# Kernel tuning notes

Hardware: AMD Instinct MI355X
Metric: run time of the kernel (lower is better)

## Reference

```python
import jax, jax.numpy as jnp
from jax import lax
import numpy as np

N_E = 1024
E_DIM = 512
BETA = 0.25


def setup_inputs() -> dict:
    key = jax.random.key(0)
    k1, k2 = jax.random.split(key)
    z = jax.random.normal(k1, (16, 4096, E_DIM), dtype=jnp.float32)
    # torch init: uniform(-1/n_e, 1/n_e)
    codebook = jax.random.uniform(k2, (N_E, E_DIM), dtype=jnp.float32,
                                  minval=-1.0 / N_E, maxval=1.0 / N_E)
    return {"z": z, "codebook": codebook}


def reference(z, codebook):
    zf = z.reshape(-1, z.shape[-1])                      # (N, e_dim)
    # squared-distance matrix: ||z||^2 + ||e||^2 - 2 z e^T  -> (N, n_e)
    d = (jnp.sum(zf * zf, axis=1, keepdims=True)
         + jnp.sum(codebook * codebook, axis=1)
         - 2.0 * (zf @ codebook.T))
    idx = jnp.argmin(d, axis=1)                          # (N,)
    z_q = codebook[idx].reshape(z.shape)                 # (B, S, e_dim)
    loss = (jnp.mean((z_q - lax.stop_gradient(z)) ** 2)
            + BETA * jnp.mean((lax.stop_gradient(z_q) - z) ** 2))
    # straight-through estimator
    z_q_st = z + lax.stop_gradient(z_q - z)
    # perplexity of code usage (mean of one-hot == normalized counts)
    counts = jnp.zeros((codebook.shape[0],), dtype=z.dtype).at[idx].add(1.0)
    e_mean = counts / idx.shape[0]
    perplexity = jnp.exp(-jnp.sum(e_mean * jnp.log(e_mean + 1e-10)))
    return (loss, z_q_st, idx, perplexity)
```

## Files before the change

### kernel.cpp

```cpp
#include <hip/hip_runtime.h>
#include <hip/hip_bf16.h>

#define N_ROWS 65536
#define EDIM   512
#define NCODES 1024

#define WS_LOSS   0
#define WS_COUNTS 1
#define WS_ENORM  1025
#define WS_ZNORM  2049
#define WS_AMBCNT (2049 + 65536)
#define WS_WINNER (WS_AMBCNT + 1)
#define WS_AMBLST (WS_WINNER + 65536)
#define AMB_CAP   32768
#define WS_E2_OFF (1u << 20)
#define WS_FAST_BYTES (3u * 1024u * 1024u + 4096u)

#define AMB_EPS 1.6e-4f

typedef short short8 __attribute__((ext_vector_type(8)));
typedef float f32x4  __attribute__((ext_vector_type(4)));

#define AS1C(p) ((const __attribute__((address_space(1))) void*)(p))
#define AS3(p)  ((__attribute__((address_space(3))) void*)(p))

static __device__ __forceinline__ unsigned short f2bf(float f) {
    unsigned u = __float_as_uint(f);
    u += 0x7FFFu + ((u >> 16) & 1u);
    return (unsigned short)(u >> 16);
}
static __device__ __forceinline__ float bf2f(unsigned short h) {
    return __uint_as_float(((unsigned)h) << 16);
}

__global__ __launch_bounds__(256) void vq_prep(const float* __restrict__ cb,
                                               float* __restrict__ ws) {
    int j = blockIdx.x;
    int tid = threadIdx.x;
    float2 v = *(const float2*)&cb[(size_t)j * EDIM + tid * 2];
    float s = v.x * v.x + v.y * v.y;
    #pragma unroll
    for (int off = 32; off > 0; off >>= 1) s += __shfl_down(s, off);
    __shared__ float ls[4];
    int wave = tid >> 6, lane = tid & 63;
    if (lane == 0) ls[wave] = s;
    __syncthreads();
    if (tid == 0) {
        ws[WS_ENORM + j] = ls[0] + ls[1] + ls[2] + ls[3];
        ws[WS_COUNTS + j] = 0.0f;
        if (j == 0) {
            ws[WS_LOSS] = 0.0f;
            ((int*)ws)[WS_AMBCNT] = 0;
        }
    }
}

__global__ __launch_bounds__(256) void vq_znorm(const float* __restrict__ z,
                                                float* __restrict__ ws) {
    int tid  = threadIdx.x;
    int lrow = tid >> 5;
    int c    = tid & 31;
    long row = (long)blockIdx.x * 8 + lrow;
    const float* p = z + row * EDIM + (c >> 3) * 128 + (c & 7);
    float r = p[0] * p[0];
    #pragma unroll
    for (int i = 1; i < 16; ++i) {
        float v = p[i * 8];
        r += v * v;
    }
    r += __shfl_xor(r, 1);
    r += __shfl_xor(r, 2);
    r += __shfl_xor(r, 4);
    r += __shfl_xor(r, 8);
    r += __shfl_xor(r, 16);
    if (c == 0) ws[WS_ZNORM + row] = r;
}

__global__ __launch_bounds__(256) void vq_convz(const float* __restrict__ z,
                                                unsigned short* __restrict__ z2) {
    const int tid = threadIdx.x;
    const int p = blockIdx.x;
    const long row0 = (long)p * 128;
    const int row = tid >> 1, half = tid & 1;
    for (int kc = 0; kc < 16; ++kc) {
        const float* src = z + (row0 + row) * EDIM + kc * 32 + half * 16;
        float f[16];
        #pragma unroll
        for (int q = 0; q < 4; ++q) {
            float4 v = ((const float4*)src)[q];
            f[q*4+0] = v.x; f[q*4+1] = v.y; f[q*4+2] = v.z; f[q*4+3] = v.w;
        }
        unsigned hi[8], lo[8];
        #pragma unroll
        for (int q = 0; q < 8; ++q) {
            unsigned short h0 = f2bf(f[2*q]);
            unsigned short h1 = f2bf(f[2*q+1]);
            unsigned short l0 = f2bf(f[2*q]   - bf2f(h0));
            unsigned short l1 = f2bf(f[2*q+1] - bf2f(h1));
            hi[q] = (unsigned)h0 | ((unsigned)h1 << 16);
            lo[q] = (unsigned)l0 | ((unsigned)l1 << 16);
        }
        size_t base = ((size_t)(p * 16 + kc) * 2) * 4096;
        unsigned* dhi = (unsigned*)(z2 + base        + row * 32 + half * 16);
        unsigned* dlo = (unsigned*)(z2 + base + 4096 + row * 32 + half * 16);
        ((uint4*)dhi)[0] = make_uint4(hi[0], hi[1], hi[2], hi[3]);
        ((uint4*)dhi)[1] = make_uint4(hi[4], hi[5], hi[6], hi[7]);
        ((uint4*)dlo)[0] = make_uint4(lo[0], lo[1], lo[2], lo[3]);
        ((uint4*)dlo)[1] = make_uint4(lo[4], lo[5], lo[6], lo[7]);
    }
}

__global__ __launch_bounds__(256) void vq_convcb(const float* __restrict__ cb,
                                                 unsigned short* __restrict__ e2) {
    const int tid = threadIdx.x;
    const int cc = blockIdx.x;
    const int row = tid >> 1, half = tid & 1;
    for (int kc = 0; kc < 16; ++kc) {
        const float* src = cb + (size_t)(cc * 128 + row) * EDIM + kc * 32 + half * 16;
        float f[16];
        #pragma unroll
        for (int q = 0; q < 4; ++q) {
            float4 v = ((const float4*)src)[q];
            f[q*4+0] = v.x; f[q*4+1] = v.y; f[q*4+2] = v.z; f[q*4+3] = v.w;
        }
        unsigned hi[8], lo[8];
        #pragma unroll
        for (int q = 0; q < 8; ++q) {
            unsigned short h0 = f2bf(f[2*q]);
            unsigned short h1 = f2bf(f[2*q+1]);
            unsigned short l0 = f2bf(f[2*q]   - bf2f(h0));
            unsigned short l1 = f2bf(f[2*q+1] - bf2f(h1));
            hi[q] = (unsigned)h0 | ((unsigned)h1 << 16);
            lo[q] = (unsigned)l0 | ((unsigned)l1 << 16);
        }
        size_t base = ((size_t)(cc * 16 + kc) * 2) * 4096;
        unsigned* dhi = (unsigned*)(e2 + base        + row * 32 + half * 16);
        unsigned* dlo = (unsigned*)(e2 + base + 4096 + row * 32 + half * 16);
        ((uint4*)dhi)[0] = make_uint4(hi[0], hi[1], hi[2], hi[3]);
        ((uint4*)dhi)[1] = make_uint4(hi[4], hi[5], hi[6], hi[7]);
        ((uint4*)dlo)[0] = make_uint4(lo[0], lo[1], lo[2], lo[3]);
        ((uint4*)dlo)[1] = make_uint4(lo[4], lo[5], lo[6], lo[7]);
    }
}

__device__ __forceinline__ void stage32(const char* zs, const char* es,
                                        char* db, int goff, int w) {
    const int wb = w << 10;
    #pragma unroll
    for (int i = 0; i < 4; ++i) {
        __builtin_amdgcn_global_load_lds(AS1C(zs + goff + i * 2048),
                                         AS3(db + i * 4096 + wb), 16, 0, 0);
        __builtin_amdgcn_global_load_lds(AS1C(es + goff + i * 2048),
                                         AS3(db + 16384 + i * 4096 + wb), 16, 0, 0);
    }
}

__global__ __launch_bounds__(256, 2) void vq_mfma(const unsigned short* __restrict__ z2,
                                                  const unsigned short* __restrict__ e2,
                                                  const float* __restrict__ ws,
                                                  int* __restrict__ winner,
                                                  int* __restrict__ amb_count,
                                                  int* __restrict__ amb_list) {
    __shared__ __attribute__((aligned(16))) char sb[2][32768];
    __shared__ float enorm_lds[NCODES];
    __shared__ float fv1[2][128];
    __shared__ float fv2[2][128];
    __shared__ int   fc1[2][128];

    const int tid  = threadIdx.x;
    const int lane = tid & 63, w = tid >> 6;
    const int rw   = (w & 1) * 64;
    const int wcol = w >> 1;
    const int cw   = wcol * 64;
    const int ml = lane & 15, kg = lane >> 4;
    const long row0 = (long)blockIdx.x * 128;

    const int t3 = tid >> 3;
    const int sl = (tid & 7) ^ (t3 & 7);
    const int goff = t3 * 64 + (sl & 3) * 16 + (sl >> 2) * 8192;

    const int xr = ml & 7;
    const int o0 = (kg ^ xr) * 16;
    const int o1 = ((4 + kg) ^ xr) * 16;
    const int za = (rw + ml) * 128;
    const int ea = 16384 + (cw + ml) * 128;

    #pragma unroll
    for (int i = 0; i < 4; ++i) enorm_lds[tid + i * 256] = ws[WS_ENORM + tid + i * 256];

    float v1[16], v2[16];
    int   c1[16];
    #pragma unroll
    for (int i = 0; i < 16; ++i) { v1[i] = INFINITY; v2[i] = INFINITY; c1[i] = 0; }

    const char* z2b = (const char*)z2 + (size_t)blockIdx.x * 16 * 16384;
    const char* e2b = (const char*)e2;

    f32x4 acc[4][4];
    #pragma unroll
    for (int rt = 0; rt < 4; ++rt)
        #pragma unroll
        for (int ct = 0; ct < 4; ++ct)
            acc[rt][ct] = (f32x4){0.f, 0.f, 0.f, 0.f};

    stage32(z2b, e2b, sb[0], goff, w);
    __syncthreads();

    int cur = 0;
    #pragma unroll 2
    for (int s = 0; s < 128; ++s) {
        if (s + 1 < 128) {
            const int s2 = s + 1;
            stage32(z2b + (size_t)(s2 & 15) * 16384,
                    e2b + (size_t)s2 * 16384,
                    sb[cur ^ 1], goff, w);
        }
        const char* bz = sb[cur];
        short8 a[4][2], b[4][2];
        #pragma unroll
        for (int rt = 0; rt < 4; ++rt) {
            a[rt][0] = *(const short8*)(bz + za + rt * 2048 + o0);
            a[rt][1] = *(const short8*)(bz + za + rt * 2048 + o1);
        }
        #pragma unroll
        for (int ct = 0; ct < 4; ++ct) {
            b[ct][0] = *(const short8*)(bz + ea + ct * 2048 + o0);
            b[ct][1] = *(const short8*)(bz + ea + ct * 2048 + o1);
        }
        #pragma unroll
        for (int rt = 0; rt < 4; ++rt)
            #pragma unroll
            for (int ct = 0; ct < 4; ++ct) {
                acc[rt][ct] = __builtin_amdgcn_mfma_f32_16x16x32_bf16(a[rt][0], b[ct][0], acc[rt][ct], 0, 0, 0);
                acc[rt][ct] = __builtin_amdgcn_mfma_f32_16x16x32_bf16(a[rt][0], b[ct][1], acc[rt][ct], 0, 0, 0);
                acc[rt][ct] = __builtin_amdgcn_mfma_f32_16x16x32_bf16(a[rt][1], b[ct][0], acc[rt][ct], 0, 0, 0);
            }
        asm volatile("s_waitcnt vmcnt(0)" ::: "memory");
        __builtin_amdgcn_s_barrier();
        asm volatile("" ::: "memory");
        cur ^= 1;

        if ((s & 15) == 15) {
            const int cc = s >> 4;
            #pragma unroll
            for (int ct = 0; ct < 4; ++ct) {
                const int code = cc * 128 + cw + ct * 16 + ml;
                const float en = enorm_lds[code];
                #pragma unroll
                for (int rt = 0; rt < 4; ++rt)
                    #pragma unroll
                    for (int reg = 0; reg < 4; ++reg) {
                        float d = fmaf(-2.0f, acc[rt][ct][reg], en);
                        int i = rt * 4 + reg;
                        bool lt1 = d < v1[i];
                        bool lt2 = d < v2[i];
                        v2[i] = lt1 ? v1[i] : (lt2 ? d : v2[i]);
                        v1[i] = lt1 ? d : v1[i];
                        c1[i] = lt1 ? code : c1[i];
                    }
            }
            #pragma unroll
            for (int rt = 0; rt < 4; ++rt)
                #pragma unroll
                for (int ct = 0; ct < 4; ++ct)
                    acc[rt][ct] = (f32x4){0.f, 0.f, 0.f, 0.f};
        }
    }

    #pragma unroll
    for (int i = 0; i < 16; ++i) {
        #pragma unroll
        for (int off = 1; off < 16; off <<= 1) {
            float ov1 = __shfl_xor(v1[i], off);
            int   oc1 = __shfl_xor(c1[i], off);
            float ov2 = __shfl_xor(v2[i], off);
            bool take = (ov1 < v1[i]) || (ov1 == v1[i] && oc1 < c1[i]);
            float nv2 = take ? fminf(v1[i], ov2) : fminf(v2[i], ov1);
            v1[i] = take ? ov1 : v1[i];
            c1[i] = take ? oc1 : c1[i];
            v2[i] = nv2;
        }
    }
    __syncthreads();
    if (ml == 0) {
        #pragma unroll
        for (int i = 0; i < 16; ++i) {
            int row = rw + (i >> 2) * 16 + kg * 4 + (i & 3);
            fv1[wcol][row] = v1[i];
            fv2[wcol][row] = v2[i];
            fc1[wcol][row] = c1[i];
        }
    }
    __syncthreads();
    if (tid < 128) {
        float a1 = fv1[0][tid], a2 = fv2[0][tid];
        int   ac = fc1[0][tid];
        float b1 = fv1[1][tid], b2 = fv2[1][tid];
        int   bc = fc1[1][tid];
        bool take = (b1 < a1) || (b1 == a1 && bc < ac);
        float V1 = take ? b1 : a1;
        int   C1 = take ? bc : ac;
        float V2 = take ? fminf(a1, b2) : fminf(a2, b1);
        winner[row0 + tid] = C1;
        if (V2 - V1 < AMB_EPS) {
            int p = atomicAdd(amb_count, 1);
            if (p < AMB_CAP) amb_list[p] = (int)(row0 + tid);
        }
    }
}

#define RB 8
#define ZSR 9
__global__ __launch_bounds__(256) void vq_recheck(const float* __restrict__ z,
                                                  const float* __restrict__ cb,
                                                  const float* __restrict__ ws,
                                                  int* __restrict__ winner,
                                                  const int* __restrict__ amb_count,
                                                  const int* __restrict__ amb_list) {
    __shared__ float zs[EDIM * ZSR];
    __shared__ float wred_d[4];
    __shared__ int   wred_i[4];
    const int tid = threadIdx.x;
    const int lane = tid & 63, wv = tid >> 6;
    const float* __restrict__ enorm = ws + WS_ENORM;

    int n = *amb_count;
    bool overflow = (n > AMB_CAP);
    if (overflow) n = N_ROWS;
    int nIter = (n + RB - 1) / RB;

    const float* ec[4];
    float en4[4];
    #pragma unroll
    for (int c = 0; c < 4; ++c) {
        ec[c]  = cb + (size_t)(tid + 256 * c) * EDIM;
        en4[c] = enorm[tid + 256 * c];
    }

    for (int ii = blockIdx.x; ii < nIter; ii += gridDim.x) {
        int rows[RB];
        #pragma unroll
        for (int j = 0; j < RB; ++j) {
            int idx = ii * RB + j;
            if (idx >= n) idx = n - 1;
            rows[j] = overflow ? idx : amb_list[idx];
        }
        __syncthreads();
        #pragma unroll
        for (int j = 0; j < RB; ++j) {
            float2 v = *(const float2*)&z[(long)rows[j] * EDIM + tid * 2];
            zs[(tid * 2 + 0) * ZSR + j] = v.x;
            zs[(tid * 2 + 1) * ZSR + j] = v.y;
        }
        __syncthreads();

        float acc[RB][4];
        #pragma unroll
        for (int r = 0; r < RB; ++r)
            #pragma unroll
            for (int c = 0; c < 4; ++c) acc[r][c] = 0.0f;

        for (int k0 = 0; k0 < EDIM; k0 += 32) {
            float ain[RB][4];
            #pragma unroll
            for (int r = 0; r < RB; ++r)
                #pragma unroll
                for (int c = 0; c < 4; ++c) ain[r][c] = 0.0f;
            #pragma unroll
            for (int ks = 0; ks < 32; ks += 8) {
                float er[4][8];
                #pragma unroll
                for (int c = 0; c < 4; ++c) {
                    float4 a = *(const float4*)&ec[c][k0 + ks];
                    float4 b = *(const float4*)&ec[c][k0 + ks + 4];
                    er[c][0]=a.x; er[c][1]=a.y; er[c][2]=a.z; er[c][3]=a.w;
                    er[c][4]=b.x; er[c][5]=b.y; er[c][6]=b.z; er[c][7]=b.w;
                }
                #pragma unroll
                for (int kk = 0; kk < 8; ++kk) {
                    const float* zp = &zs[(k0 + ks + kk) * ZSR];
                    float4 z0 = *(const float4*)zp;
                    float4 z1 = *(const float4*)(zp + 4);
                    float zr[RB] = {z0.x, z0.y, z0.z, z0.w, z1.x, z1.y, z1.z, z1.w};
                    #pragma unroll
                    for (int r = 0; r < RB; ++r)
                        #pragma unroll
                        for (int c = 0; c < 4; ++c)
                            ain[r][c] = fmaf(zr[r], er[c][kk], ain[r][c]);
                }
            }
            #pragma unroll
            for (int r = 0; r < RB; ++r)
                #pragma unroll
                for (int c = 0; c < 4; ++c) acc[r][c] += ain[r][c];
        }

        #pragma unroll
        for (int r = 0; r < RB; ++r) {
            float zn = ws[WS_ZNORM + rows[r]];
            float bd = INFINITY;
            int   bc = 0;
            #pragma unroll
            for (int c = 0; c < 4; ++c) {
                float t = zn + en4[c];
                float d = t - 2.0f * acc[r][c];
                if (d < bd) { bd = d; bc = tid + 256 * c; }
            }
            #pragma unroll
            for (int off = 1; off < 64; off <<= 1) {
                float od = __shfl_xor(bd, off);
                int   oi = __shfl_xor(bc, off);
                if (od < bd || (od == bd && oi < bc)) { bd = od; bc = oi; }
            }
            if (lane == 0) { wred_d[wv] = bd; wred_i[wv] = bc; }
            __syncthreads();
            if (tid == 0) {
                float fd = wred_d[0]; int fi = wred_i[0];
                #pragma unroll
                for (int t2 = 1; t2 < 4; ++t2) {
                    if (wred_d[t2] < fd || (wred_d[t2] == fd && wred_i[t2] < fi)) {
                        fd = wred_d[t2]; fi = wred_i[t2];
                    }
                }
                winner[rows[r]] = fi;
            }
            __syncthreads();
        }
    }
}

__global__ __launch_bounds__(256) void vq_emit(const float* __restrict__ z,
                                               const float* __restrict__ cb,
                                               const int* __restrict__ winner,
                                               float* __restrict__ ws,
                                               float* __restrict__ out_zq,
                                               float* __restrict__ out_idx) {
    __shared__ float lred[4];
    const int tid = threadIdx.x;
    const long row0 = (long)blockIdx.x * 128;
    if (tid < 128) {
        int wi = winner[row0 + tid];
        out_idx[row0 + tid] = (float)wi;
        atomicAdd(&ws[WS_COUNTS + wi], 1.0f);
    }
    float lsum = 0.0f;
    for (int r = 0; r < 128; ++r) {
        int wv = winner[row0 + r];
        float2 e  = *(const float2*)&cb[(size_t)wv * EDIM + tid * 2];
        float2 zz = *(const float2*)&z[(row0 + r) * EDIM + tid * 2];
        float d0 = e.x - zz.x, d1 = e.y - zz.y;
        float2 o; o.x = zz.x + d0; o.y = zz.y + d1;
        *(float2*)&out_zq[(row0 + r) * EDIM + tid * 2] = o;
        lsum = fmaf(d0, d0, fmaf(d1, d1, lsum));
    }
    #pragma unroll
    for (int off = 32; off > 0; off >>= 1) lsum += __shfl_down(lsum, off);
    int wave = tid >> 6, lane = tid & 63;
    if (lane == 0) lred[wave] = lsum;
    __syncthreads();
    if (tid == 0) atomicAdd(&ws[WS_LOSS], lred[0] + lred[1] + lred[2] + lred[3]);
}

__global__ __launch_bounds__(1024) void vq_final(const float* __restrict__ ws,
                                                 float* __restrict__ out,
                                                 long off_perp) {
    int tid = threadIdx.x;
    float c = ws[WS_COUNTS + tid] * (1.0f / (float)N_ROWS);
    float t = c * logf(c + 1e-10f);
    #pragma unroll
    for (int off = 32; off > 0; off >>= 1) t += __shfl_down(t, off);
    __shared__ float ls[16];
    int wave = tid >> 6, lane = tid & 63;
    if (lane == 0) ls[wave] = t;
    __syncthreads();
    if (tid == 0) {
        float h = 0.0f;
        #pragma unroll
        for (int i = 0; i < 16; ++i) h += ls[i];
        out[off_perp] = expf(-h);
        out[0] = ws[WS_LOSS] * 1.25f / (float)((long)N_ROWS * EDIM);
    }
}

#define ROWS_PER_BLOCK 128
#define CODE_CHUNK     64
#define KCHUNK         32
#define ZSTRIDE        132
#define ESTRIDE        68

__global__ __launch_bounds__(256) void vq_main_fb(const float* __restrict__ z,
                                                  const float* __restrict__ cb,
                                                  float* __restrict__ ws,
                                                  float* __restrict__ out_zq,
                                                  float* __restrict__ out_idx) {
    __shared__ float zt[KCHUNK * ZSTRIDE];
    __shared__ float et[KCHUNK * ESTRIDE];
    __shared__ float red_d[ROWS_PER_BLOCK * 8];
    __shared__ int   red_i[ROWS_PER_BLOCK * 8];
    __shared__ int   winner[ROWS_PER_BLOCK];
    __shared__ float lred[4];

    const int tid = threadIdx.x;
    const int tx = tid & 7;
    const int ty = tid >> 3;
    const long row0 = (long)blockIdx.x * ROWS_PER_BLOCK;
    const float* __restrict__ enorm = ws + WS_ENORM;
    const float* __restrict__ znorm = ws + WS_ZNORM;

    float zn[4];
    #pragma unroll
    for (int i = 0; i < 4; ++i) zn[i] = znorm[row0 + ty * 4 + i];

    float best[4];
    int   bidx[4];
    #pragma unroll
    for (int i = 0; i < 4; ++i) { best[i] = INFINITY; bidx[i] = 0; }

    const int kq    = (tid & 7) * 4;
    const int rbase = tid >> 3;

    for (int c = 0; c < NCODES; c += CODE_CHUNK) {
        float acc[4][8];
        #pragma unroll
        for (int i = 0; i < 4; ++i)
            #pragma unroll
            for (int j = 0; j < 8; ++j) acc[i][j] = 0.0f;

        for (int k0 = 0; k0 < EDIM; k0 += KCHUNK) {
            __syncthreads();
            #pragma unroll
            for (int it = 0; it < 4; ++it) {
                int r = rbase + it * 32;
                float4 v = *(const float4*)&z[(row0 + r) * EDIM + k0 + kq];
                zt[(kq + 0) * ZSTRIDE + r] = v.x;
                zt[(kq + 1) * ZSTRIDE + r] = v.y;
                zt[(kq + 2) * ZSTRIDE + r] = v.z;
                zt[(kq + 3) * ZSTRIDE + r] = v.w;
            }
            #pragma unroll
            for (int it = 0; it < 2; ++it) {
                int e = rbase + it * 32;
                float4 v = *(const float4*)&cb[(size_t)(c + e) * EDIM + k0 + kq];
                et[(kq + 0) * ESTRIDE + e] = v.x;
                et[(kq + 1) * ESTRIDE + e] = v.y;
                et[(kq + 2) * ESTRIDE + e] = v.z;
                et[(kq + 3) * ESTRIDE + e] = v.w;
            }
            __syncthreads();
            float ain[4][8];
            #pragma unroll
            for (int i = 0; i < 4; ++i)
                #pragma unroll
                for (int j = 0; j < 8; ++j) ain[i][j] = 0.0f;
            #pragma unroll
            for (int kk = 0; kk < KCHUNK; ++kk) {
                float4 zv = *(const float4*)&zt[kk * ZSTRIDE + ty * 4];
                float4 e0 = *(const float4*)&et[kk * ESTRIDE + tx * 8];
                float4 e1 = *(const float4*)&et[kk * ESTRIDE + tx * 8 + 4];
                float za[4] = {zv.x, zv.y, zv.z, zv.w};
                float ea[8] = {e0.x, e0.y, e0.z, e0.w, e1.x, e1.y, e1.z, e1.w};
                #pragma unroll
                for (int i = 0; i < 4; ++i)
                    #pragma unroll
                    for (int j = 0; j < 8; ++j)
                        ain[i][j] = fmaf(za[i], ea[j], ain[i][j]);
            }
            #pragma unroll
            for (int i = 0; i < 4; ++i)
                #pragma unroll
                for (int j = 0; j < 8; ++j) acc[i][j] += ain[i][j];
        }
        #pragma unroll
        for (int j = 0; j < 8; ++j) {
            int code = c + tx * 8 + j;
            float en = enorm[code];
            #pragma unroll
            for (int i = 0; i < 4; ++i) {
                float t = zn[i] + en;
                float d = t - 2.0f * acc[i][j];
                if (d < best[i]) { best[i] = d; bidx[i] = code; }
            }
        }
    }

    __syncthreads();
    #pragma unroll
    for (int i = 0; i < 4; ++i) {
        red_d[(ty * 4 + i) * 8 + tx] = best[i];
        red_i[(ty * 4 + i) * 8 + tx] = bidx[i];
    }
    __syncthreads();
    if (tid < ROWS_PER_BLOCK) {
        float bd = red_d[tid * 8];
        int   bi = red_i[tid * 8];
        #pragma unroll
        for (int t = 1; t < 8; ++t) {
            float dv = red_d[tid * 8 + t];
            int   iv = red_i[tid * 8 + t];
            if (dv < bd || (dv == bd && iv < bi)) { bd = dv; bi = iv; }
        }
        winner[tid] = bi;
        out_idx[row0 + tid] = (float)bi;
        atomicAdd(&ws[WS_COUNTS + bi], 1.0f);
    }
    __syncthreads();

    float lsum = 0.0f;
    for (int r = 0; r < ROWS_PER_BLOCK; ++r) {
        int w = winner[r];
        float2 e  = *(const float2*)&cb[(size_t)w * EDIM + tid * 2];
        float2 zz = *(const float2*)&z[(row0 + r) * EDIM + tid * 2];
        float d0 = e.x - zz.x, d1 = e.y - zz.y;
        float2 o; o.x = zz.x + d0; o.y = zz.y + d1;
        *(float2*)&out_zq[(row0 + r) * EDIM + tid * 2] = o;
        lsum = fmaf(d0, d0, fmaf(d1, d1, lsum));
    }
    #pragma unroll
    for (int off = 32; off > 0; off >>= 1) lsum += __shfl_down(lsum, off);
    int wave = tid >> 6, lane = tid & 63;
    if (lane == 0) lred[wave] = lsum;
    __syncthreads();
    if (tid == 0) atomicAdd(&ws[WS_LOSS], lred[0] + lred[1] + lred[2] + lred[3]);
}

extern "C" void kernel_launch(void* const* d_in, const int* in_sizes, int n_in,
                              void* d_out, int out_size, void* d_ws, size_t ws_size,
                              hipStream_t stream) {
    const float* z  = (const float*)d_in[0];
    const float* cb = (const float*)d_in[1];
    float* out = (float*)d_out;
    float* ws  = (float*)d_ws;

    float* out_zq  = out + 1;
    float* out_idx = out + 1 + (long)N_ROWS * EDIM;
    long   off_perp = 1 + (long)N_ROWS * EDIM + N_ROWS;

    hipLaunchKernelGGL(vq_prep, dim3(NCODES), dim3(256), 0, stream, cb, ws);
    hipLaunchKernelGGL(vq_znorm, dim3(N_ROWS / 8), dim3(256), 0, stream, z, ws);

    if (ws_size >= (size_t)WS_FAST_BYTES) {
        unsigned short* z2 = (unsigned short*)(out + 4);
        unsigned short* e2 = (unsigned short*)((char*)d_ws + WS_E2_OFF);
        int* winner    = ((int*)ws) + WS_WINNER;
        int* amb_count = ((int*)ws) + WS_AMBCNT;
        int* amb_list  = ((int*)ws) + WS_AMBLST;

        hipLaunchKernelGGL(vq_convz, dim3(N_ROWS / 128), dim3(256), 0, stream, z, z2);
        hipLaunchKernelGGL(vq_convcb, dim3(8), dim3(256), 0, stream, cb, e2);
        hipLaunchKernelGGL(vq_mfma, dim3(N_ROWS / 128), dim3(256), 0, stream,
                           z2, e2, ws, winner, amb_count, amb_list);
        hipLaunchKernelGGL(vq_recheck, dim3(1024), dim3(256), 0, stream,
                           z, cb, ws, winner, amb_count, amb_list);
        hipLaunchKernelGGL(vq_emit, dim3(N_ROWS / 128), dim3(256), 0, stream,
                           z, cb, winner, ws, out_zq, out_idx);
    } else {
        hipLaunchKernelGGL(vq_main_fb, dim3(N_ROWS / 128), dim3(256), 0, stream,
                           z, cb, ws, out_zq, out_idx);
    }
    hipLaunchKernelGGL(vq_final, dim3(1), dim3(1024), 0, stream, ws, out, off_perp);
}
```

Before: 713.7 us.

## Enlarge MFMA distance tile to 256x256 with 512-thread blocks

The bf16-split distance GEMM block tile grows from 128 rows x 128 codes to 256 rows x 256 codes, using 8 waves each computing a 64x128 sub-tile, with 64 KB double-buffered LDS stages. Each wave loads B fragments per column tile and reuses its A fragments across 8 column tiles, raising arithmetic intensity per LDS read and halving global re-reads of the codebook and z. In exchange it uses more LDS (about 128 KB per block) and more accumulator registers, which may lower occupancy and leave fewer blocks to fill the CUs.

```diff
diff --git a/kernel.cpp b/kernel.cpp
--- a/kernel.cpp
+++ b/kernel.cpp
@@ -143,98 +143,99 @@
     }
 }
 
-__device__ __forceinline__ void stage32(const char* zs, const char* es,
-                                        char* db, int goff, int w) {
-    const int wb = w << 10;
-    #pragma unroll
-    for (int i = 0; i < 4; ++i) {
-        __builtin_amdgcn_global_load_lds(AS1C(zs + goff + i * 2048),
-                                         AS3(db + i * 4096 + wb), 16, 0, 0);
-        __builtin_amdgcn_global_load_lds(AS1C(es + goff + i * 2048),
-                                         AS3(db + 16384 + i * 4096 + wb), 16, 0, 0);
-    }
-}
-
-__global__ __launch_bounds__(256, 2) void vq_mfma(const unsigned short* __restrict__ z2,
+__device__ __forceinline__ void stage_chunk(const char* src, char* dst, int goff0,
+                                            int wb) {
+    __builtin_amdgcn_global_load_lds(AS1C(src + goff0),        AS3(dst + wb),        16, 0, 0);
+    __builtin_amdgcn_global_load_lds(AS1C(src + goff0 + 4096), AS3(dst + 8192 + wb), 16, 0, 0);
+}
+
+__device__ __forceinline__ void stage_step(const char* zb, const char* eb, char* buf,
+                                           int goff0, int wb) {
+    stage_chunk(zb,              buf,         goff0, wb);
+    stage_chunk(zb + 16 * 16384, buf + 16384, goff0, wb);
+    stage_chunk(eb,              buf + 32768, goff0, wb);
+    stage_chunk(eb + 16 * 16384, buf + 49152, goff0, wb);
+}
+
+__global__ __launch_bounds__(512, 2) void vq_mfma(const unsigned short* __restrict__ z2,
                                                   const unsigned short* __restrict__ e2,
                                                   const float* __restrict__ ws,
                                                   int* __restrict__ winner,
                                                   int* __restrict__ amb_count,
                                                   int* __restrict__ amb_list) {
-    __shared__ __attribute__((aligned(16))) char sb[2][32768];
+    __shared__ __attribute__((aligned(16))) char sb[2][65536];
     __shared__ float enorm_lds[NCODES];
-    __shared__ float fv1[2][128];
-    __shared__ float fv2[2][128];
-    __shared__ int   fc1[2][128];
+    __shared__ float fv1[2][256];
+    __shared__ float fv2[2][256];
+    __shared__ int   fc1[2][256];
 
     const int tid  = threadIdx.x;
     const int lane = tid & 63, w = tid >> 6;
-    const int rw   = (w & 1) * 64;
-    const int wcol = w >> 1;
-    const int cw   = wcol * 64;
+    const int wr   = (w & 3) * 64;
+    const int wcg  = w >> 2;
+    const int wc   = wcg * 128;
     const int ml = lane & 15, kg = lane >> 4;
-    const long row0 = (long)blockIdx.x * 128;
+    const long row0 = (long)blockIdx.x * 256;
 
     const int t3 = tid >> 3;
     const int sl = (tid & 7) ^ (t3 & 7);
-    const int goff = t3 * 64 + (sl & 3) * 16 + (sl >> 2) * 8192;
+    const int goff0 = t3 * 64 + (sl & 3) * 16 + (sl >> 2) * 8192;
+    const int wb = w << 10;
 
     const int xr = ml & 7;
     const int o0 = (kg ^ xr) * 16;
     const int o1 = ((4 + kg) ^ xr) * 16;
-    const int za = (rw + ml) * 128;
-    const int ea = 16384 + (cw + ml) * 128;
-
-    #pragma unroll
-    for (int i = 0; i < 4; ++i) enorm_lds[tid + i * 256] = ws[WS_ENORM + tid + i * 256];
+    const int za = (wr + ml) * 128;
+    const int ea = 32768 + (wc + ml) * 128;
+
+    enorm_lds[tid]       = ws[WS_ENORM + tid];
+    enorm_lds[tid + 512] = ws[WS_ENORM + tid + 512];
 
     float v1[16], v2[16];
     int   c1[16];
     #pragma unroll
     for (int i = 0; i < 16; ++i) { v1[i] = INFINITY; v2[i] = INFINITY; c1[i] = 0; }
 
-    const char* z2b = (const char*)z2 + (size_t)blockIdx.x * 16 * 16384;
+    const char* z2b = (const char*)z2 + (size_t)blockIdx.x * 2 * 16 * 16384;
     const char* e2b = (const char*)e2;
 
-    f32x4 acc[4][4];
+    f32x4 acc[4][8];
     #pragma unroll
     for (int rt = 0; rt < 4; ++rt)
         #pragma unroll
-        for (int ct = 0; ct < 4; ++ct)
+        for (int ct = 0; ct < 8; ++ct)
             acc[rt][ct] = (f32x4){0.f, 0.f, 0.f, 0.f};
 
-    stage32(z2b, e2b, sb[0], goff, w);
+    stage_step(z2b, e2b, sb[0], goff0, wb);
     __syncthreads();
 
     int cur = 0;
     #pragma unroll 2
-    for (int s = 0; s < 128; ++s) {
-        if (s + 1 < 128) {
-            const int s2 = s + 1;
-            stage32(z2b + (size_t)(s2 & 15) * 16384,
-                    e2b + (size_t)s2 * 16384,
-                    sb[cur ^ 1], goff, w);
+    for (int s = 0; s < 64; ++s) {
+        if (s + 1 < 64) {
+            const int s2 = s + 1, cc2 = s2 >> 4, kc2 = s2 & 15;
+            stage_step(z2b + (size_t)kc2 * 16384,
+                       e2b + (size_t)(cc2 * 32 + kc2) * 16384,
+                       sb[cur ^ 1], goff0, wb);
         }
         const char* bz = sb[cur];
-        short8 a[4][2], b[4][2];
+        short8 a[4][2];
         #pragma unroll
         for (int rt = 0; rt < 4; ++rt) {
             a[rt][0] = *(const short8*)(bz + za + rt * 2048 + o0);
             a[rt][1] = *(const short8*)(bz + za + rt * 2048 + o1);
         }
         #pragma unroll
-        for (int ct = 0; ct < 4; ++ct) {
-            b[ct][0] = *(const short8*)(bz + ea + ct * 2048 + o0);
-            b[ct][1] = *(const short8*)(bz + ea + ct * 2048 + o1);
-        }
-        #pragma unroll
-        for (int rt = 0; rt < 4; ++rt)
-            #pragma unroll
-            for (int ct = 0; ct < 4; ++ct) {
-                acc[rt][ct] = __builtin_amdgcn_mfma_f32_16x16x32_bf16(a[rt][0], b[ct][0], acc[rt][ct], 0, 0, 0);
-                acc[rt][ct] = __builtin_amdgcn_mfma_f32_16x16x32_bf16(a[rt][0], b[ct][1], acc[rt][ct], 0, 0, 0);
-                acc[rt][ct] = __builtin_amdgcn_mfma_f32_16x16x32_bf16(a[rt][1], b[ct][0], acc[rt][ct], 0, 0, 0);
-            }
+        for (int ct = 0; ct < 8; ++ct) {
+            short8 b0 = *(const short8*)(bz + ea + ct * 2048 + o0);
+            short8 b1 = *(const short8*)(bz + ea + ct * 2048 + o1);
+            #pragma unroll
+            for (int rt = 0; rt < 4; ++rt) {
+                acc[rt][ct] = __builtin_amdgcn_mfma_f32_16x16x32_bf16(a[rt][0], b0, acc[rt][ct], 0, 0, 0);
+                acc[rt][ct] = __builtin_amdgcn_mfma_f32_16x16x32_bf16(a[rt][0], b1, acc[rt][ct], 0, 0, 0);
+                acc[rt][ct] = __builtin_amdgcn_mfma_f32_16x16x32_bf16(a[rt][1], b0, acc[rt][ct], 0, 0, 0);
+            }
+        }
         asm volatile("s_waitcnt vmcnt(0)" ::: "memory");
         __builtin_amdgcn_s_barrier();
         asm volatile("" ::: "memory");
@@ -243,8 +244,8 @@
         if ((s & 15) == 15) {
             const int cc = s >> 4;
             #pragma unroll
-            for (int ct = 0; ct < 4; ++ct) {
-                const int code = cc * 128 + cw + ct * 16 + ml;
+            for (int ct = 0; ct < 8; ++ct) {
+                const int code = cc * 256 + wc + ct * 16 + ml;
                 const float en = enorm_lds[code];
                 #pragma unroll
                 for (int rt = 0; rt < 4; ++rt)
@@ -262,7 +263,7 @@
             #pragma unroll
             for (int rt = 0; rt < 4; ++rt)
                 #pragma unroll
-                for (int ct = 0; ct < 4; ++ct)
+                for (int ct = 0; ct < 8; ++ct)
                     acc[rt][ct] = (f32x4){0.f, 0.f, 0.f, 0.f};
         }
     }
@@ -285,14 +286,14 @@
     if (ml == 0) {
         #pragma unroll
         for (int i = 0; i < 16; ++i) {
-            int row = rw + (i >> 2) * 16 + kg * 4 + (i & 3);
-            fv1[wcol][row] = v1[i];
-            fv2[wcol][row] = v2[i];
-            fc1[wcol][row] = c1[i];
-        }
-    }
-    __syncthreads();
-    if (tid < 128) {
+            int row = wr + (i >> 2) * 16 + kg * 4 + (i & 3);
+            fv1[wcg][row] = v1[i];
+            fv2[wcg][row] = v2[i];
+            fc1[wcg][row] = c1[i];
+        }
+    }
+    __syncthreads();
+    if (tid < 256) {
         float a1 = fv1[0][tid], a2 = fv2[0][tid];
         int   ac = fc1[0][tid];
         float b1 = fv1[1][tid], b2 = fv2[1][tid];
@@ -647,7 +648,7 @@
 
         hipLaunchKernelGGL(vq_convz, dim3(N_ROWS / 128), dim3(256), 0, stream, z, z2);
         hipLaunchKernelGGL(vq_convcb, dim3(8), dim3(256), 0, stream, cb, e2);
-        hipLaunchKernelGGL(vq_mfma, dim3(N_ROWS / 128), dim3(256), 0, stream,
+        hipLaunchKernelGGL(vq_mfma, dim3(N_ROWS / 256), dim3(512), 0, stream,
                            z2, e2, ws, winner, amb_count, amb_list);
         hipLaunchKernelGGL(vq_recheck, dim3(1024), dim3(256), 0, stream,
                            z, cb, ws, winner, amb_count, amb_list);
```

After: 680.0 us. 1.05x faster.
